# Optimization experiments

Hardware: AMD Instinct MI355X
Metric: run time of the kernel (lower is better)

The kernel has to match this reference:

```python
import jax, jax.numpy as jnp
import numpy as np

N_NODES = 100000
N_EDGES = 3200000
IN_DIM = 64


def setup_inputs() -> dict:
    key = jax.random.key(0)
    k_h, k_d, k_w, k_s, k_t = jax.random.split(key, 5)
    h = jax.random.normal(k_h, (N_NODES, IN_DIM), dtype=jnp.float32)
    # degree normalizer (e.g. deg^-1/2 in FAGCN); strictly positive values
    d = jax.random.uniform(k_d, (N_NODES,), dtype=jnp.float32, minval=0.05, maxval=1.0)
    # gate: Linear(2*in_dim, 1), xavier_normal_(gain=1.414)
    gain = 1.414
    std = gain * np.sqrt(2.0 / (2 * IN_DIM + 1))
    gate_W = jax.random.normal(k_w, (1, 2 * IN_DIM), dtype=jnp.float32) * std
    gate_b = jnp.zeros((1,), dtype=jnp.float32)
    edge_src = jax.random.randint(k_s, (N_EDGES,), 0, N_NODES, dtype=jnp.int32)
    edge_dst = jax.random.randint(k_t, (N_EDGES,), 0, N_NODES, dtype=jnp.int32)
    return {"h": h, "d": d, "gate_W": gate_W, "gate_b": gate_b,
            "edge_src": edge_src, "edge_dst": edge_dst}


def reference(h, d, gate_W, gate_b, edge_src, edge_dst):
    N, D = h.shape
    # Linear on concat([h_dst, h_src]) == h_dst @ W_dst^T + h_src @ W_src^T + b.
    # Compute the two halves per-node (dense GEMV), then gather scalars per-edge
    # instead of gathering/concatenating [E, 2D] features.
    W_dst = gate_W[0, :D]   # [D]
    W_src = gate_W[0, D:]   # [D]
    gd = h @ W_dst          # [N]
    gs = h @ W_src          # [N]
    tem_g = jnp.tanh(gd[edge_dst] + gs[edge_src] + gate_b[0])   # [E]
    # e = tanh_gate * d_dst * d_src  (dropout is identity in eval / p=0)
    e = tem_g * d[edge_dst] * d[edge_src]                        # [E]
    # message passing: z[dst] += h[src] * e
    msg = h[edge_src] * e[:, None]                               # [E, D]
    z = jax.ops.segment_sum(msg, edge_dst, num_segments=N)       # [N, D]
    return z
```

## Files before the change

### kernel.cpp

```cpp
#include <hip/hip_runtime.h>
#include <hip/hip_bf16.h>

#define DIM 64
#define BKN 64
#define BKSH 6
#define MAXBK 1600
#define PCHUNK 12288
#define MAXPB 512
#define CAP 2944

__device__ inline float fast_tanh(float x) {
    float e = __expf(2.0f * x);
    return 1.0f - 2.0f / (e + 1.0f);
}

__device__ inline float4 i8x4_unpack(uint q) {
    return make_float4((float)((int)(q << 24) >> 24),
                       (float)((int)(q << 16) >> 24),
                       (float)((int)(q <<  8) >> 24),
                       (float)((int)q >> 24));
}

__global__ __launch_bounds__(1024)
void fa_place_gates(const float* __restrict__ h,
                    const float* __restrict__ gate_W,
                    const float* __restrict__ dn,
                    float2* __restrict__ gdd,
                    float4* __restrict__ gss4,
                    unsigned char* __restrict__ hq,
                    const int* __restrict__ esrc, const int* __restrict__ edst,
                    int* __restrict__ segs, int* __restrict__ lens,
                    int* __restrict__ pairs,
                    int E, int N, int nbk, int nplace) {
    __shared__ int stage[PCHUNK];
    __shared__ int lh[2048];
    __shared__ int lex[2048];
    __shared__ int wtot[16];
    int tid = threadIdx.x;
    if ((int)blockIdx.x < nplace) {
        int blk = blockIdx.x;
        int c0 = blk * PCHUNK;
        int c1 = min(E, c0 + PCHUNK);
        lh[tid] = 0; lh[tid + 1024] = 0;
        __syncthreads();
        for (int i = c0 + tid; i < c1; i += 1024) {
            int t = edst[i];
            int s = esrc[i];
            stage[i - c0] = (s << BKSH) | (t & (BKN - 1));
            atomicAdd(&lh[t >> BKSH], 1);
        }
        __syncthreads();
        int lane = tid & 63, wv = tid >> 6;
        int a0 = lh[2 * tid], a1 = lh[2 * tid + 1];
        int s = a0 + a1;
        int v = s;
        #pragma unroll
        for (int d = 1; d < 64; d <<= 1) {
            int t = __shfl_up(v, d, 64);
            if (lane >= d) v += t;
        }
        if (lane == 63) wtot[wv] = v;
        __syncthreads();
        int base = 0;
        #pragma unroll
        for (int k = 0; k < 16; ++k) base += (k < wv) ? wtot[k] : 0;
        int excl = v + base - s;
        lex[2 * tid] = excl;
        lex[2 * tid + 1] = excl + a0;
        __syncthreads();
        for (int i = tid; i < nbk; i += 1024) {
            segs[(size_t)i * MAXPB + blk] = c0 + lex[i];
            lens[(size_t)i * MAXPB + blk] = lh[i];
        }
        __syncthreads();
        for (int i = c0 + tid; i < c1; i += 1024) {
            int t = edst[i];
            int pos = c0 + atomicAdd(&lex[t >> BKSH], 1);
            pairs[pos] = stage[i - c0];
        }
    } else {
        int gid  = (blockIdx.x - nplace) * 1024 + tid;
        int node = gid >> 6;
        int lane = tid & 63;
        if (node >= N) return;
        float x = h[(size_t)node * DIM + lane];
        float a = x * gate_W[lane];
        float b = x * gate_W[DIM + lane];
        float m = fabsf(x);
        #pragma unroll
        for (int off = 32; off >= 1; off >>= 1) {
            a += __shfl_xor(a, off, 64);
            b += __shfl_xor(b, off, 64);
            m = fmaxf(m, __shfl_xor(m, off, 64));
        }
        float inv = (m > 0.f) ? (127.0f / m) : 0.f;
        int q = __float2int_rn(x * inv);
        int s0 = __shfl(q, (lane << 2) + 0, 64);
        int s1 = __shfl(q, (lane << 2) + 1, 64);
        int s2 = __shfl(q, (lane << 2) + 2, 64);
        int s3 = __shfl(q, (lane << 2) + 3, 64);
        if (lane < 16) {
            uint packed = (uint)(s0 & 0xff) | ((uint)(s1 & 0xff) << 8)
                        | ((uint)(s2 & 0xff) << 16) | ((uint)(s3 & 0xff) << 24);
            ((uint*)hq)[(size_t)node * 16 + lane] = packed;
        }
        if (lane == 0) {
            float dv = dn[node];
            gdd[node]  = make_float2(a, dv);
            gss4[node] = make_float4(b, dv, m / 127.0f, 0.f);
        }
    }
}

__global__ void fa_node_gates(const float* __restrict__ h,
                              const float* __restrict__ gate_W,
                              const float* __restrict__ dn,
                              float2* __restrict__ gdd,
                              float4* __restrict__ gss4,
                              int N) {
    int gid  = blockIdx.x * blockDim.x + threadIdx.x;
    int node = gid >> 6;
    int lane = threadIdx.x & 63;
    if (node >= N) return;
    float x = h[(size_t)node * DIM + lane];
    float a = x * gate_W[lane];
    float b = x * gate_W[DIM + lane];
    #pragma unroll
    for (int off = 32; off >= 1; off >>= 1) {
        a += __shfl_xor(a, off, 64);
        b += __shfl_xor(b, off, 64);
    }
    if (lane == 0) {
        float dv = dn[node];
        gdd[node]  = make_float2(a, dv);
        gss4[node] = make_float4(b, dv, 0.f, 0.f);
    }
}

__global__ __launch_bounds__(512, 4)
void fa_gather11(const unsigned char* __restrict__ hq,
                 const float2* __restrict__ gdd, const float4* __restrict__ gss4,
                 const float* __restrict__ gate_b,
                 const int* __restrict__ segs, const int* __restrict__ lens,
                 const int* __restrict__ pairs,
                 float* __restrict__ z, int N, int nbk, int nplace) {
    __shared__ int  stg[CAP];
    __shared__ int2 buf2[CAP];
    __shared__ int  sc[512];
    __shared__ int  wtot[8];
    __shared__ float2 gdl[BKN];
    __shared__ int hist[BKN];
    __shared__ int cur[BKN];
    __shared__ int offl[BKN + 1];
    int b   = blockIdx.x;
    int q8  = nbk >> 3, r8 = nbk & 7;
    int xcd = b & 7, idx = b >> 3;
    int bk  = (xcd < r8 ? xcd * (q8 + 1) : r8 * (q8 + 1) + (xcd - r8) * q8) + idx;
    int tid = threadIdx.x;
    int n0  = bk << BKSH;
    int wid  = tid >> 6;
    int lane = tid & 63;
    float gb = gate_b[0];
    const int* segrow = segs + (size_t)bk * MAXPB;
    const int* lenrow = lens + (size_t)bk * MAXPB;
    int ll = (tid < nplace) ? lenrow[tid] : 0;
    if (tid < BKN) {
        int node = n0 + tid;
        gdl[tid]  = (node < N) ? gdd[node] : make_float2(0.f, 0.f);
        hist[tid] = 0;
    }
    int v = ll;
    #pragma unroll
    for (int d = 1; d < 64; d <<= 1) {
        int t = __shfl_up(v, d, 64);
        if (lane >= d) v += t;
    }
    if (lane == 63) wtot[wid] = v;
    __syncthreads();
    int base = 0, c = 0;
    #pragma unroll
    for (int k = 0; k < 8; ++k) {
        base += (k < wid) ? wtot[k] : 0;
        c    += wtot[k];
    }
    sc[tid] = v + base;
    __syncthreads();
    if (c <= CAP) {
        int qid = lane >> 4;
        int l16 = lane & 15;
        for (int sp = (wid << 2) + qid; sp < nplace; sp += 32) {
            int ll2 = lenrow[sp];
            int ss2 = segrow[sp];
            int ex  = sc[sp] - ll2;
            for (int k = l16; k < ll2; k += 16) {
                int r = pairs[ss2 + k];
                stg[ex + k] = r;
                atomicAdd(&hist[r & (BKN - 1)], 1);
            }
        }
        __syncthreads();
        if (tid < BKN) {
            int hv = hist[tid];
            int v2 = hv;
            #pragma unroll
            for (int d = 1; d < BKN; d <<= 1) {
                int t = __shfl_up(v2, d, 64);
                if (tid >= d) v2 += t;
            }
            offl[tid + 1] = v2;
            cur[tid] = v2 - hv;
            if (tid == 0) offl[0] = 0;
        }
        __syncthreads();
        for (int i = tid; i < c; i += 512) {
            int r  = stg[i];
            int lt = r & (BKN - 1);
            int s  = r >> BKSH;
            float4 bs = gss4[s];
            float2 ad = gdl[lt];
            float g  = fast_tanh(ad.x + bs.x + gb);
            float ev = g * ad.y * bs.y * bs.z;
            int p = atomicAdd(&cur[lt], 1);
            buf2[p] = make_int2(s, __float_as_int(ev));
        }
        __syncthreads();
        for (int ln = wid; ln < BKN; ln += 8) {
            int node = n0 + ln;
            if (node >= N) break;
            int j   = offl[ln];
            int end = offl[ln + 1];
            float4 a0 = make_float4(0.f, 0.f, 0.f, 0.f);
            float4 a1 = a0, a2 = a0, a3 = a0;
            for (; j + 16 <= end; j += 16) {
                int2 p0 = buf2[j + qid];
                int2 p1 = buf2[j + qid + 4];
                int2 p2 = buf2[j + qid + 8];
                int2 p3 = buf2[j + qid + 12];
                uint q0 = ((const uint*)(hq + (size_t)p0.x * DIM))[l16];
                uint q1 = ((const uint*)(hq + (size_t)p1.x * DIM))[l16];
                uint q2 = ((const uint*)(hq + (size_t)p2.x * DIM))[l16];
                uint q3 = ((const uint*)(hq + (size_t)p3.x * DIM))[l16];
                float e0 = __int_as_float(p0.y);
                float e1 = __int_as_float(p1.y);
                float e2 = __int_as_float(p2.y);
                float e3 = __int_as_float(p3.y);
                float4 h0 = i8x4_unpack(q0);
                float4 h1 = i8x4_unpack(q1);
                float4 h2 = i8x4_unpack(q2);
                float4 h3 = i8x4_unpack(q3);
                a0.x += h0.x * e0; a0.y += h0.y * e0; a0.z += h0.z * e0; a0.w += h0.w * e0;
                a1.x += h1.x * e1; a1.y += h1.y * e1; a1.z += h1.z * e1; a1.w += h1.w * e1;
                a2.x += h2.x * e2; a2.y += h2.y * e2; a2.z += h2.z * e2; a2.w += h2.w * e2;
                a3.x += h3.x * e3; a3.y += h3.y * e3; a3.z += h3.z * e3; a3.w += h3.w * e3;
            }
            for (; j + 4 <= end; j += 4) {
                int2 p = buf2[j + qid];
                uint q = ((const uint*)(hq + (size_t)p.x * DIM))[l16];
                float e = __int_as_float(p.y);
                float4 hv = i8x4_unpack(q);
                a0.x += hv.x * e; a0.y += hv.y * e; a0.z += hv.z * e; a0.w += hv.w * e;
            }
            int rem = end - j;
            if (rem > 0) {
                int idx2 = j + (qid < rem ? qid : 0);
                int2 p = buf2[idx2];
                float e = (qid < rem) ? __int_as_float(p.y) : 0.f;
                uint q = ((const uint*)(hq + (size_t)p.x * DIM))[l16];
                float4 hv = i8x4_unpack(q);
                a0.x += hv.x * e; a0.y += hv.y * e; a0.z += hv.z * e; a0.w += hv.w * e;
            }
            float4 t;
            t.x = a0.x + a1.x + a2.x + a3.x;
            t.y = a0.y + a1.y + a2.y + a3.y;
            t.z = a0.z + a1.z + a2.z + a3.z;
            t.w = a0.w + a1.w + a2.w + a3.w;
            t.x += __shfl_xor(t.x, 16, 64);  t.x += __shfl_xor(t.x, 32, 64);
            t.y += __shfl_xor(t.y, 16, 64);  t.y += __shfl_xor(t.y, 32, 64);
            t.z += __shfl_xor(t.z, 16, 64);  t.z += __shfl_xor(t.z, 32, 64);
            t.w += __shfl_xor(t.w, 16, 64);  t.w += __shfl_xor(t.w, 32, 64);
            if (qid == 0)
                *(float4*)&z[(size_t)node * DIM + (l16 << 2)] = t;
        }
    } else {
        for (int ln = wid; ln < BKN; ln += 8) {
            int node = n0 + ln;
            if (node >= N) break;
            float2 ad = gdl[ln];
            float acc = 0.f;
            for (int sp = 0; sp < nplace; ++sp) {
                int ss2 = segrow[sp];
                int ll2 = lenrow[sp];
                for (int i = 0; i < ll2; ++i) {
                    int r = pairs[ss2 + i];
                    if ((r & (BKN - 1)) == ln) {
                        int s = r >> BKSH;
                        float4 bs = gss4[s];
                        float g  = fast_tanh(ad.x + bs.x + gb);
                        uint qw = ((const uint*)(hq + (size_t)s * DIM))[lane >> 2];
                        int qv = (int)(qw << ((3 - (lane & 3)) * 8)) >> 24;
                        acc += (float)qv * (g * ad.y * bs.y * bs.z);
                    }
                }
            }
            z[(size_t)node * DIM + lane] = acc;
        }
    }
}

__global__ void fa_edge_scatter_atomic(const float* __restrict__ h,
                                       const float2* __restrict__ gdd,
                                       const float4* __restrict__ gss4,
                                       const int* __restrict__ esrc,
                                       const int* __restrict__ edst,
                                       const float* __restrict__ gate_b,
                                       float* __restrict__ z, int E) {
    int gid  = blockIdx.x * blockDim.x + threadIdx.x;
    int edge = gid >> 6;
    int lane = threadIdx.x & 63;
    if (edge >= E) return;
    int s = esrc[edge];
    int t = edst[edge];
    float2 ad = gdd[t];
    float4 bs = gss4[s];
    float g  = fast_tanh(ad.x + bs.x + gate_b[0]);
    float ev = g * ad.y * bs.y;
    atomicAdd(&z[(size_t)t * DIM + lane], h[(size_t)s * DIM + lane] * ev);
}

extern "C" void kernel_launch(void* const* d_in, const int* in_sizes, int n_in,
                              void* d_out, int out_size, void* d_ws, size_t ws_size,
                              hipStream_t stream) {
    const float* h      = (const float*)d_in[0];
    const float* dn     = (const float*)d_in[1];
    const float* gate_W = (const float*)d_in[2];
    const float* gate_b = (const float*)d_in[3];
    const int*   esrc   = (const int*)d_in[4];
    const int*   edst   = (const int*)d_in[5];
    float*       z      = (float*)d_out;

    int N = in_sizes[1];
    int E = in_sizes[4];
    int nbk    = (N + BKN - 1) >> BKSH;
    int nplace = (E + PCHUNK - 1) / PCHUNK;

    char* w = (char*)d_ws;
    float2* gdd  = (float2*)w;         w += (size_t)N * 8;
    float4* gss4 = (float4*)w;         w += (size_t)N * 16;
    int*   segs  = (int*)w;            w += (size_t)MAXBK * MAXPB * 4;
    int*   lens  = (int*)w;            w += (size_t)MAXBK * MAXPB * 4;
    w = (char*)(((uintptr_t)w + 63) & ~(uintptr_t)63);
    int*  pairs  = (int*)w;            w += ((size_t)E + 64) * 4;
    unsigned char* hq = (unsigned char*)w;
    w += (size_t)N * DIM;
    size_t required = (size_t)(w - (char*)d_ws);
    size_t atomic_required = (size_t)N * 24;

    bool use_sort = (ws_size >= required) && (nbk <= MAXBK) && (nplace <= MAXPB);

    if (use_sort) {
        int gatesBlocks = (N + 15) / 16;
        fa_place_gates<<<nplace + gatesBlocks, 1024, 0, stream>>>(
            h, gate_W, dn, gdd, gss4, hq, esrc, edst, segs, lens, pairs,
            E, N, nbk, nplace);
        fa_gather11<<<nbk, 512, 0, stream>>>(hq, gdd, gss4, gate_b, segs, lens,
                                             pairs, z, N, nbk, nplace);
    } else if (ws_size >= atomic_required) {
        fa_node_gates<<<(N + 3) / 4, 256, 0, stream>>>(h, gate_W, dn, gdd, gss4, N);
        hipMemsetAsync(z, 0, (size_t)out_size * sizeof(float), stream);
        fa_edge_scatter_atomic<<<(E + 3) / 4, 256, 0, stream>>>(h, gdd, gss4, esrc,
                                                                edst, gate_b, z, E);
    }
}
```

Before: 123.3 us.

## Pack segment offsets and lengths into block-major int2 table; vectorize gate/quantize pass

Segment starts and lengths go into a single int2 table indexed by place block, then bucket. Each place block now writes one contiguous row instead of two strided columns. The gather kernel loads its column once into shared memory and gets lengths from the prefix-scan differences, so the per-segment global reads go away. Separately, the node-gate and quantize path now uses 16 lanes per node with float4 loads, which cuts the cross-lane shuffles and lets each block cover 64 nodes. The cost is that the gather's initial column read is strided across rows.

```diff
diff --git a/kernel.cpp b/kernel.cpp
--- a/kernel.cpp
+++ b/kernel.cpp
@@ -29,7 +29,7 @@
                     float4* __restrict__ gss4,
                     unsigned char* __restrict__ hq,
                     const int* __restrict__ esrc, const int* __restrict__ edst,
-                    int* __restrict__ segs, int* __restrict__ lens,
+                    int2* __restrict__ seglen,
                     int* __restrict__ pairs,
                     int E, int N, int nbk, int nplace) {
     __shared__ int stage[PCHUNK];
@@ -68,10 +68,9 @@
         lex[2 * tid] = excl;
         lex[2 * tid + 1] = excl + a0;
         __syncthreads();
-        for (int i = tid; i < nbk; i += 1024) {
-            segs[(size_t)i * MAXPB + blk] = c0 + lex[i];
-            lens[(size_t)i * MAXPB + blk] = lh[i];
-        }
+        int2* row = seglen + (size_t)blk * MAXBK;
+        for (int i = tid; i < nbk; i += 1024)
+            row[i] = make_int2(c0 + lex[i], lh[i]);
         __syncthreads();
         for (int i = c0 + tid; i < c1; i += 1024) {
             int t = edst[i];
@@ -79,32 +78,33 @@
             pairs[pos] = stage[i - c0];
         }
     } else {
-        int gid  = (blockIdx.x - nplace) * 1024 + tid;
-        int node = gid >> 6;
+        int base_node = (blockIdx.x - nplace) * 64;
+        int wv   = tid >> 6;
         int lane = tid & 63;
+        int l16  = lane & 15;
+        int node = base_node + (wv << 2) + (lane >> 4);
         if (node >= N) return;
-        float x = h[(size_t)node * DIM + lane];
-        float a = x * gate_W[lane];
-        float b = x * gate_W[DIM + lane];
-        float m = fabsf(x);
+        float4 x4 = ((const float4*)h)[(size_t)node * 16 + l16];
+        float4 w0 = ((const float4*)gate_W)[l16];
+        float4 w1 = ((const float4*)gate_W)[16 + l16];
+        float a = x4.x * w0.x + x4.y * w0.y + x4.z * w0.z + x4.w * w0.w;
+        float b = x4.x * w1.x + x4.y * w1.y + x4.z * w1.z + x4.w * w1.w;
+        float m = fmaxf(fmaxf(fabsf(x4.x), fabsf(x4.y)),
+                        fmaxf(fabsf(x4.z), fabsf(x4.w)));
         #pragma unroll
-        for (int off = 32; off >= 1; off >>= 1) {
-            a += __shfl_xor(a, off, 64);
-            b += __shfl_xor(b, off, 64);
-            m = fmaxf(m, __shfl_xor(m, off, 64));
+        for (int off = 1; off < 16; off <<= 1) {
+            a += __shfl_xor(a, off, 16);
+            b += __shfl_xor(b, off, 16);
+            m = fmaxf(m, __shfl_xor(m, off, 16));
         }
         float inv = (m > 0.f) ? (127.0f / m) : 0.f;
-        int q = __float2int_rn(x * inv);
-        int s0 = __shfl(q, (lane << 2) + 0, 64);
-        int s1 = __shfl(q, (lane << 2) + 1, 64);
-        int s2 = __shfl(q, (lane << 2) + 2, 64);
-        int s3 = __shfl(q, (lane << 2) + 3, 64);
-        if (lane < 16) {
-            uint packed = (uint)(s0 & 0xff) | ((uint)(s1 & 0xff) << 8)
-                        | ((uint)(s2 & 0xff) << 16) | ((uint)(s3 & 0xff) << 24);
-            ((uint*)hq)[(size_t)node * 16 + lane] = packed;
-        }
-        if (lane == 0) {
+        int q0 = __float2int_rn(x4.x * inv) & 0xff;
+        int q1 = __float2int_rn(x4.y * inv) & 0xff;
+        int q2 = __float2int_rn(x4.z * inv) & 0xff;
+        int q3 = __float2int_rn(x4.w * inv) & 0xff;
+        ((uint*)hq)[(size_t)node * 16 + l16] =
+            (uint)q0 | ((uint)q1 << 8) | ((uint)q2 << 16) | ((uint)q3 << 24);
+        if (l16 == 0) {
             float dv = dn[node];
             gdd[node]  = make_float2(a, dv);
             gss4[node] = make_float4(b, dv, m / 127.0f, 0.f);
@@ -138,10 +138,10 @@
 }
 
 __global__ __launch_bounds__(512, 4)
-void fa_gather11(const unsigned char* __restrict__ hq,
+void fa_gather12(const unsigned char* __restrict__ hq,
                  const float2* __restrict__ gdd, const float4* __restrict__ gss4,
                  const float* __restrict__ gate_b,
-                 const int* __restrict__ segs, const int* __restrict__ lens,
+                 const int2* __restrict__ seglen,
                  const int* __restrict__ pairs,
                  float* __restrict__ z, int N, int nbk, int nplace) {
     __shared__ int  stg[CAP];
@@ -161,9 +161,9 @@
     int wid  = tid >> 6;
     int lane = tid & 63;
     float gb = gate_b[0];
-    const int* segrow = segs + (size_t)bk * MAXPB;
-    const int* lenrow = lens + (size_t)bk * MAXPB;
-    int ll = (tid < nplace) ? lenrow[tid] : 0;
+    int2 sl = (tid < nplace) ? seglen[(size_t)tid * MAXBK + bk] : make_int2(0, 0);
+    ((int*)buf2)[tid] = sl.x;
+    int ll = sl.y;
     if (tid < BKN) {
         int node = n0 + tid;
         gdl[tid]  = (node < N) ? gdd[node] : make_float2(0.f, 0.f);
@@ -189,12 +189,13 @@
         int qid = lane >> 4;
         int l16 = lane & 15;
         for (int sp = (wid << 2) + qid; sp < nplace; sp += 32) {
-            int ll2 = lenrow[sp];
-            int ss2 = segrow[sp];
-            int ex  = sc[sp] - ll2;
+            int inc  = sc[sp];
+            int prev = (sp == 0) ? 0 : sc[sp - 1];
+            int ll2  = inc - prev;
+            int ss2  = ((int*)buf2)[sp];
             for (int k = l16; k < ll2; k += 16) {
                 int r = pairs[ss2 + k];
-                stg[ex + k] = r;
+                stg[prev + k] = r;
                 atomicAdd(&hist[r & (BKN - 1)], 1);
             }
         }
@@ -288,10 +289,9 @@
             float2 ad = gdl[ln];
             float acc = 0.f;
             for (int sp = 0; sp < nplace; ++sp) {
-                int ss2 = segrow[sp];
-                int ll2 = lenrow[sp];
-                for (int i = 0; i < ll2; ++i) {
-                    int r = pairs[ss2 + i];
+                int2 sl2 = seglen[(size_t)sp * MAXBK + bk];
+                for (int i = 0; i < sl2.y; ++i) {
+                    int r = pairs[sl2.x + i];
                     if ((r & (BKN - 1)) == ln) {
                         int s = r >> BKSH;
                         float4 bs = gss4[s];
@@ -346,9 +346,8 @@
     char* w = (char*)d_ws;
     float2* gdd  = (float2*)w;         w += (size_t)N * 8;
     float4* gss4 = (float4*)w;         w += (size_t)N * 16;
-    int*   segs  = (int*)w;            w += (size_t)MAXBK * MAXPB * 4;
-    int*   lens  = (int*)w;            w += (size_t)MAXBK * MAXPB * 4;
     w = (char*)(((uintptr_t)w + 63) & ~(uintptr_t)63);
+    int2*  seglen = (int2*)w;          w += (size_t)MAXPB * MAXBK * 8;
     int*  pairs  = (int*)w;            w += ((size_t)E + 64) * 4;
     unsigned char* hq = (unsigned char*)w;
     w += (size_t)N * DIM;
@@ -358,11 +357,11 @@
     bool use_sort = (ws_size >= required) && (nbk <= MAXBK) && (nplace <= MAXPB);
 
     if (use_sort) {
-        int gatesBlocks = (N + 15) / 16;
+        int gatesBlocks = (N + 63) / 64;
         fa_place_gates<<<nplace + gatesBlocks, 1024, 0, stream>>>(
-            h, gate_W, dn, gdd, gss4, hq, esrc, edst, segs, lens, pairs,
+            h, gate_W, dn, gdd, gss4, hq, esrc, edst, seglen, pairs,
             E, N, nbk, nplace);
-        fa_gather11<<<nbk, 512, 0, stream>>>(hq, gdd, gss4, gate_b, segs, lens,
+        fa_gather12<<<nbk, 512, 0, stream>>>(hq, gdd, gss4, gate_b, seglen,
                                              pairs, z, N, nbk, nplace);
     } else if (ws_size >= atomic_required) {
         fa_node_gates<<<(N + 3) / 4, 256, 0, stream>>>(h, gate_W, dn, gdd, gss4, N);
```

Result: faster. 104.4 us, median of 2 (-15.3%).
